# Kernel optimization log

Hardware: AMD Instinct MI355X
Metric: run time of the kernel (lower is better)

## Reference

```python
import jax, jax.numpy as jnp
import numpy as np

B, T, I, H, O = 256, 100, 1024, 2048, 10

def setup_inputs() -> dict:
    key = jax.random.key(0)
    k = jax.random.split(key, 6)
    return {
        "x": jax.random.normal(k[0], (B, T, I), dtype=jnp.float32),
        "h0": jax.random.normal(k[1], (B, H), dtype=jnp.float32),
        "Win": jax.random.uniform(k[2], (I, H), dtype=jnp.float32, minval=-0.1, maxval=0.1),
        "W": jax.random.normal(k[3], (H, H), dtype=jnp.float32) * 0.01,
        "lin_w": jax.random.normal(k[4], (O, H), dtype=jnp.float32) * 0.02,
        "lin_b": jax.random.normal(k[5], (O,), dtype=jnp.float32) * 0.02,
    }

def reference(x, h0, Win, W, lin_w, lin_b):
    xin = jnp.einsum('bti,ih->bth', x, Win)  # precompute input projection for all steps

    def step(h, xin_t):
        h = jnp.tanh(xin_t + h @ W)
        y = h @ lin_w.T + lin_b
        return h, y

    _, ys = jax.lax.scan(step, h0, jnp.swapaxes(xin, 0, 1))  # ys: [T, B, O]
    return jnp.swapaxes(ys, 0, 1)  # [B, T, O]
```

## Files before the change

### kernel.cpp

```cpp
#include <hip/hip_runtime.h>
#include <math.h>

#define Bn 256
#define Tn 100
#define In 1024
#define Hn 2048
#define On 10
#define Kc (In + Hn)

typedef short s8v  __attribute__((ext_vector_type(8)));
typedef unsigned short us4 __attribute__((ext_vector_type(4)));
typedef float f32x4 __attribute__((ext_vector_type(4)));

__device__ __forceinline__ unsigned short f2bf(float f) {
    unsigned int u = __float_as_uint(f);
    u += 0x7fffu + ((u >> 16) & 1u);
    return (unsigned short)(u >> 16);
}

__device__ __forceinline__ float fast_tanh(float x) {
    float e = __expf(x + x);
    return 1.0f - 2.0f * __builtin_amdgcn_rcpf(e + 1.0f);
}


__global__ void conv_x_kernel(const float4* __restrict__ src, ushort4* __restrict__ dst) {
    int i = blockIdx.x * 256 + threadIdx.x;
    float4 v = src[i];
    ushort4 o;
    o.x = f2bf(v.x); o.y = f2bf(v.y); o.z = f2bf(v.z); o.w = f2bf(v.w);
    dst[i] = o;
}

__global__ void transpose_bf16_kernel(const float* __restrict__ src, unsigned short* __restrict__ dst,
                                      int N, int ld, int colOff) {
    __shared__ float tile[32][33];
    int k0 = blockIdx.x * 32;
    int n0 = blockIdx.y * 32;
    int c = threadIdx.x & 31;
    int r = threadIdx.x >> 5;
    #pragma unroll
    for (int i = 0; i < 32; i += 8)
        tile[r + i][c] = src[(size_t)(k0 + r + i) * N + n0 + c];
    __syncthreads();
    #pragma unroll
    for (int i = 0; i < 32; i += 8)
        dst[(size_t)(n0 + r + i) * ld + colOff + k0 + c] = f2bf(tile[c][r + i]);
}

__global__ void small_conv_kernel(const float* __restrict__ h0, const float* __restrict__ lin_w,
                                  unsigned short* __restrict__ h_all0, unsigned short* __restrict__ lwb,
                                  unsigned int* __restrict__ bar) {
    int idx = blockIdx.x * 256 + threadIdx.x;
    if (idx < 512) bar[idx] = 0u;
    if (idx < Bn * Hn) {
        h_all0[idx] = f2bf(h0[idx]);
    } else {
        int j = idx - Bn * Hn;
        int o = j >> 11;
        int k = j & 2047;
        lwb[j] = (o < On) ? f2bf(lin_w[o * Hn + k]) : (unsigned short)0;
    }
}

__global__ __launch_bounds__(512, 2)
void scan_kernel(const unsigned short* __restrict__ xb,
                 const unsigned short* __restrict__ BTm,
                 unsigned short* __restrict__ h_all,
                 unsigned int* __restrict__ bar) {
    const int g = blockIdx.x;
    const int mg = (g & 7) >> 1;
    const int m0 = mg * 64;
    const int n0 = ((g >> 3) * 2 + (g & 1)) * 32;
    const int w = threadIdx.x >> 6;
    const int lane = threadIdx.x & 63;
    const int quad = lane >> 4;
    const int lr = lane & 15;

    __shared__ float red[8][64][36];

    const unsigned short* bp0 = BTm + (size_t)(n0 + lr) * Kc;
    const unsigned short* bp1 = BTm + (size_t)(n0 + 16 + lr) * Kc;

    const size_t xrow = (size_t)Tn * In;

    const int fidx = mg * 64 + (g & 1) * 32 + (g >> 3);
    unsigned int* fl = bar + mg * 64;

    s8v bx[4][2];
    s8v bh[8][2];
    #pragma unroll
    for (int c = 0; c < 4; ++c) {
        const int kq = w * 128 + c * 32 + quad * 8;
        bx[c][0] = *(const s8v*)(bp0 + kq);
        bx[c][1] = *(const s8v*)(bp1 + kq);
    }
    #pragma unroll
    for (int c = 0; c < 8; ++c) {
        const int kq = In + w * 256 + c * 32 + quad * 8;
        bh[c][0] = *(const s8v*)(bp0 + kq);
        bh[c][1] = *(const s8v*)(bp1 + kq);
    }

    f32x4 acc[4][2];
    #pragma unroll
    for (int mi = 0; mi < 4; ++mi)
        #pragma unroll
        for (int ni = 0; ni < 2; ++ni)
            acc[mi][ni] = (f32x4){0.f, 0.f, 0.f, 0.f};

    {
        const unsigned short* xt = xb + 0 * In;
        #pragma unroll
        for (int c = 0; c < 4; ++c) {
            const int kq = w * 128 + c * 32 + quad * 8;
            const unsigned short* arow = xt + kq + (size_t)(m0 + lr) * xrow;
            s8v a0 = *(const s8v*)(arow);
            s8v a1 = *(const s8v*)(arow + 16 * xrow);
            s8v a2 = *(const s8v*)(arow + 32 * xrow);
            s8v a3 = *(const s8v*)(arow + 48 * xrow);
            acc[0][0] = __builtin_amdgcn_mfma_f32_16x16x32_bf16(a0, bx[c][0], acc[0][0], 0, 0, 0);
            acc[1][0] = __builtin_amdgcn_mfma_f32_16x16x32_bf16(a1, bx[c][0], acc[1][0], 0, 0, 0);
            acc[2][0] = __builtin_amdgcn_mfma_f32_16x16x32_bf16(a2, bx[c][0], acc[2][0], 0, 0, 0);
            acc[3][0] = __builtin_amdgcn_mfma_f32_16x16x32_bf16(a3, bx[c][0], acc[3][0], 0, 0, 0);
            acc[0][1] = __builtin_amdgcn_mfma_f32_16x16x32_bf16(a0, bx[c][1], acc[0][1], 0, 0, 0);
            acc[1][1] = __builtin_amdgcn_mfma_f32_16x16x32_bf16(a1, bx[c][1], acc[1][1], 0, 0, 0);
            acc[2][1] = __builtin_amdgcn_mfma_f32_16x16x32_bf16(a2, bx[c][1], acc[2][1], 0, 0, 0);
            acc[3][1] = __builtin_amdgcn_mfma_f32_16x16x32_bf16(a3, bx[c][1], acc[3][1], 0, 0, 0);
        }
    }

    for (int t = 0; t < Tn; ++t) {
        const unsigned short* hrow = h_all + (size_t)t * (Bn * Hn)
                                   + (size_t)(m0 + lr) * Hn + w * 256 + quad * 8;
        s8v A[2][4];
        #pragma unroll
        for (int r = 0; r < 4; ++r)
            A[0][r] = *(const s8v*)(hrow + r * 16 * Hn);
        #pragma unroll
        for (int c = 0; c < 8; ++c) {
            if (c < 7) {
                const unsigned short* p = hrow + (c + 1) * 32;
                #pragma unroll
                for (int r = 0; r < 4; ++r)
                    A[(c + 1) & 1][r] = *(const s8v*)(p + r * 16 * Hn);
            }
            const s8v a0 = A[c & 1][0];
            const s8v a1 = A[c & 1][1];
            const s8v a2 = A[c & 1][2];
            const s8v a3 = A[c & 1][3];
            acc[0][0] = __builtin_amdgcn_mfma_f32_16x16x32_bf16(a0, bh[c][0], acc[0][0], 0, 0, 0);
            acc[1][0] = __builtin_amdgcn_mfma_f32_16x16x32_bf16(a1, bh[c][0], acc[1][0], 0, 0, 0);
            acc[2][0] = __builtin_amdgcn_mfma_f32_16x16x32_bf16(a2, bh[c][0], acc[2][0], 0, 0, 0);
            acc[3][0] = __builtin_amdgcn_mfma_f32_16x16x32_bf16(a3, bh[c][0], acc[3][0], 0, 0, 0);
            acc[0][1] = __builtin_amdgcn_mfma_f32_16x16x32_bf16(a0, bh[c][1], acc[0][1], 0, 0, 0);
            acc[1][1] = __builtin_amdgcn_mfma_f32_16x16x32_bf16(a1, bh[c][1], acc[1][1], 0, 0, 0);
            acc[2][1] = __builtin_amdgcn_mfma_f32_16x16x32_bf16(a2, bh[c][1], acc[2][1], 0, 0, 0);
            acc[3][1] = __builtin_amdgcn_mfma_f32_16x16x32_bf16(a3, bh[c][1], acc[3][1], 0, 0, 0);
        }

        #pragma unroll
        for (int mi = 0; mi < 4; ++mi)
            #pragma unroll
            for (int ni = 0; ni < 2; ++ni)
                #pragma unroll
                for (int rr = 0; rr < 4; ++rr)
                    red[w][mi * 16 + quad * 4 + rr][ni * 16 + lr] = acc[mi][ni][rr];
        __syncthreads();

        {
            int j = threadIdx.x << 2;
            int row = j >> 5;
            int c0 = j & 31;
            float4 s0 = *(const float4*)&red[0][row][c0];
            float4 s1 = *(const float4*)&red[1][row][c0];
            float4 s2 = *(const float4*)&red[2][row][c0];
            float4 s3 = *(const float4*)&red[3][row][c0];
            float4 s4 = *(const float4*)&red[4][row][c0];
            float4 s5 = *(const float4*)&red[5][row][c0];
            float4 s6 = *(const float4*)&red[6][row][c0];
            float4 s7 = *(const float4*)&red[7][row][c0];
            us4 o4;
            o4[0] = f2bf(fast_tanh(((s0.x + s1.x) + (s2.x + s3.x)) + ((s4.x + s5.x) + (s6.x + s7.x))));
            o4[1] = f2bf(fast_tanh(((s0.y + s1.y) + (s2.y + s3.y)) + ((s4.y + s5.y) + (s6.y + s7.y))));
            o4[2] = f2bf(fast_tanh(((s0.z + s1.z) + (s2.z + s3.z)) + ((s4.z + s5.z) + (s6.z + s7.z))));
            o4[3] = f2bf(fast_tanh(((s0.w + s1.w) + (s2.w + s3.w)) + ((s4.w + s5.w) + (s6.w + s7.w))));
            unsigned long long* dst = (unsigned long long*)
                (h_all + (size_t)(t + 1) * (Bn * Hn) + (size_t)(m0 + row) * Hn + n0 + c0);
            __hip_atomic_store(dst, __builtin_bit_cast(unsigned long long, o4),
                               __ATOMIC_RELAXED, __HIP_MEMORY_SCOPE_AGENT);
        }

        if (t < Tn - 1) {
            __syncthreads();
            const unsigned int tp1 = (unsigned int)(t + 1);

            if (threadIdx.x == 0)
                __hip_atomic_store(bar + fidx, tp1, __ATOMIC_RELAXED,
                                   __HIP_MEMORY_SCOPE_AGENT);

            #pragma unroll
            for (int mi = 0; mi < 4; ++mi)
                #pragma unroll
                for (int ni = 0; ni < 2; ++ni)
                    acc[mi][ni] = (f32x4){0.f, 0.f, 0.f, 0.f};
            const unsigned short* xt = xb + (size_t)(t + 1) * In;
            #pragma unroll
            for (int c = 0; c < 4; ++c) {
                const int kq = w * 128 + c * 32 + quad * 8;
                const unsigned short* arow = xt + kq + (size_t)(m0 + lr) * xrow;
                s8v a0 = *(const s8v*)(arow);
                s8v a1 = *(const s8v*)(arow + 16 * xrow);
                s8v a2 = *(const s8v*)(arow + 32 * xrow);
                s8v a3 = *(const s8v*)(arow + 48 * xrow);
                acc[0][0] = __builtin_amdgcn_mfma_f32_16x16x32_bf16(a0, bx[c][0], acc[0][0], 0, 0, 0);
                acc[1][0] = __builtin_amdgcn_mfma_f32_16x16x32_bf16(a1, bx[c][0], acc[1][0], 0, 0, 0);
                acc[2][0] = __builtin_amdgcn_mfma_f32_16x16x32_bf16(a2, bx[c][0], acc[2][0], 0, 0, 0);
                acc[3][0] = __builtin_amdgcn_mfma_f32_16x16x32_bf16(a3, bx[c][0], acc[3][0], 0, 0, 0);
                acc[0][1] = __builtin_amdgcn_mfma_f32_16x16x32_bf16(a0, bx[c][1], acc[0][1], 0, 0, 0);
                acc[1][1] = __builtin_amdgcn_mfma_f32_16x16x32_bf16(a1, bx[c][1], acc[1][1], 0, 0, 0);
                acc[2][1] = __builtin_amdgcn_mfma_f32_16x16x32_bf16(a2, bx[c][1], acc[2][1], 0, 0, 0);
                acc[3][1] = __builtin_amdgcn_mfma_f32_16x16x32_bf16(a3, bx[c][1], acc[3][1], 0, 0, 0);
            }

            while (true) {
                unsigned int v = __hip_atomic_load(fl + lane, __ATOMIC_RELAXED,
                                                   __HIP_MEMORY_SCOPE_AGENT);
                if (__all((int)(v >= tp1))) break;
                __builtin_amdgcn_s_sleep(1);
            }
            asm volatile("" ::: "memory");
        }
    }
}

__global__ __launch_bounds__(256)
void gemm2_kernel(const unsigned short* __restrict__ h_all, const unsigned short* __restrict__ lwb,
                  const float* __restrict__ lb, float* __restrict__ y) {
    int gw = blockIdx.x * 4 + (threadIdx.x >> 6);
    int lane = threadIdx.x & 63, quad = lane >> 4, lr = lane & 15;
    int m0 = gw * 16;
    int t = m0 >> 8;
    int b0 = m0 & 255;
    const unsigned short* ah = h_all + ((size_t)(t + 1) * Bn + b0 + lr) * Hn + quad * 8;
    const unsigned short* bh = lwb + (size_t)lr * Hn + quad * 8;
    f32x4 acc0 = {0.f, 0.f, 0.f, 0.f}, acc1 = {0.f, 0.f, 0.f, 0.f};
    #pragma unroll
    for (int k0 = 0; k0 < Hn; k0 += 64) {
        s8v a0 = *(const s8v*)(ah + k0);
        s8v b0 = *(const s8v*)(bh + k0);
        acc0 = __builtin_amdgcn_mfma_f32_16x16x32_bf16(a0, b0, acc0, 0, 0, 0);
        s8v a1 = *(const s8v*)(ah + k0 + 32);
        s8v b1 = *(const s8v*)(bh + k0 + 32);
        acc1 = __builtin_amdgcn_mfma_f32_16x16x32_bf16(a1, b1, acc1, 0, 0, 0);
    }
    acc0 = acc0 + acc1;
    if (lr < On) {
        float bias = lb[lr];
        #pragma unroll
        for (int rr = 0; rr < 4; ++rr) {
            int b = b0 + quad * 4 + rr;
            y[(size_t)b * (Tn * On) + t * On + lr] = acc0[rr] + bias;
        }
    }
}


extern "C" void kernel_launch(void* const* d_in, const int* in_sizes, int n_in,
                              void* d_out, int out_size, void* d_ws, size_t ws_size,
                              hipStream_t stream) {
    const float* x   = (const float*)d_in[0];
    const float* h0  = (const float*)d_in[1];
    const float* Win = (const float*)d_in[2];
    const float* W   = (const float*)d_in[3];
    const float* lw  = (const float*)d_in[4];
    const float* lb  = (const float*)d_in[5];
    float* y = (float*)d_out;

    unsigned short* ws    = (unsigned short*)d_ws;
    unsigned short* xb    = ws;
    unsigned short* BTm   = xb + (size_t)Bn * Tn * In;
    unsigned short* h_all = BTm + (size_t)Hn * Kc;
    unsigned short* lwb   = h_all + (size_t)(Tn + 1) * Bn * Hn;
    unsigned int*   bar   = (unsigned int*)(lwb + 32768);

    conv_x_kernel<<<25600, 256, 0, stream>>>((const float4*)x, (ushort4*)xb);
    transpose_bf16_kernel<<<dim3(32, 64), 256, 0, stream>>>(Win, BTm, Hn, Kc, 0);
    transpose_bf16_kernel<<<dim3(64, 64), 256, 0, stream>>>(W, BTm, Hn, Kc, In);
    small_conv_kernel<<<2176, 256, 0, stream>>>(h0, lw, h_all, lwb, bar);

    scan_kernel<<<256, 512, 0, stream>>>(xb, BTm, h_all, bar);

    gemm2_kernel<<<400, 256, 0, stream>>>(h_all, lwb, lb, y);
}
```

Before: 1.378 ms.

## Stagger K-chunk order per block, prefetch next x tile, single-wave barrier polling

Rotates the K-chunk traversal order per N-block (hoff/xoff) so that blocks reading the same h and x rows start at different addresses, spreading memory-channel traffic. Issues half of the next step's x loads before the LDS reduction barrier so their latency overlaps the reduction and tanh. Replaces the __syncthreads with a raw s_barrier that waits only on LDS. The grid barrier is now polled by wave 0 alone, and a workgroup barrier releases the other waves. This adds register pressure for the prefetched X tiles. It also relies on the raw barrier's memory semantics being enough for ordering the relaxed loads of h.

```diff
diff --git a/kernel.cpp b/kernel.cpp
--- a/kernel.cpp
+++ b/kernel.cpp
@@ -71,11 +71,14 @@
     const int g = blockIdx.x;
     const int mg = (g & 7) >> 1;
     const int m0 = mg * 64;
-    const int n0 = ((g >> 3) * 2 + (g & 1)) * 32;
+    const int nIdx = (g >> 3) * 2 + (g & 1);
+    const int n0 = nIdx * 32;
     const int w = threadIdx.x >> 6;
     const int lane = threadIdx.x & 63;
     const int quad = lane >> 4;
     const int lr = lane & 15;
+    const int hoff = nIdx & 7;
+    const int xoff = nIdx & 3;
 
     __shared__ float red[8][64][36];
 
@@ -91,13 +94,13 @@
     s8v bh[8][2];
     #pragma unroll
     for (int c = 0; c < 4; ++c) {
-        const int kq = w * 128 + c * 32 + quad * 8;
+        const int kq = w * 128 + (((c + xoff) & 3) * 32) + quad * 8;
         bx[c][0] = *(const s8v*)(bp0 + kq);
         bx[c][1] = *(const s8v*)(bp1 + kq);
     }
     #pragma unroll
     for (int c = 0; c < 8; ++c) {
-        const int kq = In + w * 256 + c * 32 + quad * 8;
+        const int kq = In + w * 256 + (((c + hoff) & 7) * 32) + quad * 8;
         bh[c][0] = *(const s8v*)(bp0 + kq);
         bh[c][1] = *(const s8v*)(bp1 + kq);
     }
@@ -110,11 +113,10 @@
             acc[mi][ni] = (f32x4){0.f, 0.f, 0.f, 0.f};
 
     {
-        const unsigned short* xt = xb + 0 * In;
+        const unsigned short* ar0 = xb + (size_t)(m0 + lr) * xrow + w * 128 + quad * 8;
         #pragma unroll
         for (int c = 0; c < 4; ++c) {
-            const int kq = w * 128 + c * 32 + quad * 8;
-            const unsigned short* arow = xt + kq + (size_t)(m0 + lr) * xrow;
+            const unsigned short* arow = ar0 + ((c + xoff) & 3) * 32;
             s8v a0 = *(const s8v*)(arow);
             s8v a1 = *(const s8v*)(arow + 16 * xrow);
             s8v a2 = *(const s8v*)(arow + 32 * xrow);
@@ -136,11 +138,11 @@
         s8v A[2][4];
         #pragma unroll
         for (int r = 0; r < 4; ++r)
-            A[0][r] = *(const s8v*)(hrow + r * 16 * Hn);
+            A[0][r] = *(const s8v*)(hrow + hoff * 32 + r * 16 * Hn);
         #pragma unroll
         for (int c = 0; c < 8; ++c) {
             if (c < 7) {
-                const unsigned short* p = hrow + (c + 1) * 32;
+                const unsigned short* p = hrow + ((c + 1 + hoff) & 7) * 32;
                 #pragma unroll
                 for (int r = 0; r < 4; ++r)
                     A[(c + 1) & 1][r] = *(const s8v*)(p + r * 16 * Hn);
@@ -166,7 +168,24 @@
                 #pragma unroll
                 for (int rr = 0; rr < 4; ++rr)
                     red[w][mi * 16 + quad * 4 + rr][ni * 16 + lr] = acc[mi][ni][rr];
-        __syncthreads();
+
+        s8v X[2][4];
+        const unsigned short* arn = xb + (size_t)(t + 1) * In
+                                  + (size_t)(m0 + lr) * xrow + w * 128 + quad * 8;
+        if (t < Tn - 1) {
+            #pragma unroll
+            for (int c = 0; c < 2; ++c) {
+                const unsigned short* p = arn + ((c + xoff) & 3) * 32;
+                #pragma unroll
+                for (int r = 0; r < 4; ++r)
+                    X[c][r] = *(const s8v*)(p + r * 16 * xrow);
+            }
+        }
+
+        __builtin_amdgcn_sched_barrier(0);
+        asm volatile("s_waitcnt lgkmcnt(0)" ::: "memory");
+        __builtin_amdgcn_s_barrier();
+        __builtin_amdgcn_sched_barrier(0);
 
         {
             int j = threadIdx.x << 2;
@@ -204,15 +223,24 @@
                 #pragma unroll
                 for (int ni = 0; ni < 2; ++ni)
                     acc[mi][ni] = (f32x4){0.f, 0.f, 0.f, 0.f};
-            const unsigned short* xt = xb + (size_t)(t + 1) * In;
-            #pragma unroll
-            for (int c = 0; c < 4; ++c) {
-                const int kq = w * 128 + c * 32 + quad * 8;
-                const unsigned short* arow = xt + kq + (size_t)(m0 + lr) * xrow;
-                s8v a0 = *(const s8v*)(arow);
-                s8v a1 = *(const s8v*)(arow + 16 * xrow);
-                s8v a2 = *(const s8v*)(arow + 32 * xrow);
-                s8v a3 = *(const s8v*)(arow + 48 * xrow);
+            #pragma unroll
+            for (int c = 0; c < 2; ++c) {
+                acc[0][0] = __builtin_amdgcn_mfma_f32_16x16x32_bf16(X[c][0], bx[c][0], acc[0][0], 0, 0, 0);
+                acc[1][0] = __builtin_amdgcn_mfma_f32_16x16x32_bf16(X[c][1], bx[c][0], acc[1][0], 0, 0, 0);
+                acc[2][0] = __builtin_amdgcn_mfma_f32_16x16x32_bf16(X[c][2], bx[c][0], acc[2][0], 0, 0, 0);
+                acc[3][0] = __builtin_amdgcn_mfma_f32_16x16x32_bf16(X[c][3], bx[c][0], acc[3][0], 0, 0, 0);
+                acc[0][1] = __builtin_amdgcn_mfma_f32_16x16x32_bf16(X[c][0], bx[c][1], acc[0][1], 0, 0, 0);
+                acc[1][1] = __builtin_amdgcn_mfma_f32_16x16x32_bf16(X[c][1], bx[c][1], acc[1][1], 0, 0, 0);
+                acc[2][1] = __builtin_amdgcn_mfma_f32_16x16x32_bf16(X[c][2], bx[c][1], acc[2][1], 0, 0, 0);
+                acc[3][1] = __builtin_amdgcn_mfma_f32_16x16x32_bf16(X[c][3], bx[c][1], acc[3][1], 0, 0, 0);
+            }
+            #pragma unroll
+            for (int c = 2; c < 4; ++c) {
+                const unsigned short* p = arn + ((c + xoff) & 3) * 32;
+                s8v a0 = *(const s8v*)(p);
+                s8v a1 = *(const s8v*)(p + 16 * xrow);
+                s8v a2 = *(const s8v*)(p + 32 * xrow);
+                s8v a3 = *(const s8v*)(p + 48 * xrow);
                 acc[0][0] = __builtin_amdgcn_mfma_f32_16x16x32_bf16(a0, bx[c][0], acc[0][0], 0, 0, 0);
                 acc[1][0] = __builtin_amdgcn_mfma_f32_16x16x32_bf16(a1, bx[c][0], acc[1][0], 0, 0, 0);
                 acc[2][0] = __builtin_amdgcn_mfma_f32_16x16x32_bf16(a2, bx[c][0], acc[2][0], 0, 0, 0);
@@ -223,13 +251,17 @@
                 acc[3][1] = __builtin_amdgcn_mfma_f32_16x16x32_bf16(a3, bx[c][1], acc[3][1], 0, 0, 0);
             }
 
-            while (true) {
-                unsigned int v = __hip_atomic_load(fl + lane, __ATOMIC_RELAXED,
-                                                   __HIP_MEMORY_SCOPE_AGENT);
-                if (__all((int)(v >= tp1))) break;
-                __builtin_amdgcn_s_sleep(1);
+            if (w == 0) {
+                while (true) {
+                    unsigned int v = __hip_atomic_load(fl + lane, __ATOMIC_RELAXED,
+                                                       __HIP_MEMORY_SCOPE_AGENT);
+                    if (__all((int)(v >= tp1))) break;
+                    __builtin_amdgcn_s_sleep(1);
+                }
             }
             asm volatile("" ::: "memory");
+            __builtin_amdgcn_s_barrier();
+            __builtin_amdgcn_sched_barrier(0);
         }
     }
 }
```

After: 1.313 ms. 1.05x faster.
